# Kernel optimization log

Hardware: AMD Instinct MI355X
Metric: run time of the kernel (lower is better)

Reference implementation:

```python
import jax, jax.numpy as jnp
import numpy as np

B, D, L, N = 16, 256, 4096, 4096
MAX_SPAN = 64


def setup_inputs() -> dict:
    key = jax.random.key(0)
    k1, k2, k3 = jax.random.split(key, 3)
    features = jax.random.normal(k1, (B, D, L), dtype=jnp.float32)
    # TOI spans: start in [0, L - MAX_SPAN), length in [1, MAX_SPAN]
    start = jax.random.randint(k2, (B, N), 0, L - MAX_SPAN, dtype=jnp.int32)
    length = jax.random.randint(k3, (B, N), 1, MAX_SPAN + 1, dtype=jnp.int32)
    tois = jnp.stack([start, start + length], axis=-1)  # [B, N, 2]
    return {"features": features, "tois": tois}


def _pool_one(feat, toi):
    # feat: [D, L], toi: [N, 2] -> [N, 3*D]
    start = toi[:, 0]
    end = toi[:, 1]
    # cumsum with zero-padding column: [D, L+1]
    cs = jnp.concatenate(
        [jnp.zeros((feat.shape[0], 1), dtype=feat.dtype), jnp.cumsum(feat, axis=1)],
        axis=1,
    )
    span_len = (end - start).astype(feat.dtype)
    avg = (cs[:, end] - cs[:, start]) / span_len          # [D, N]
    head = feat[:, start]                                  # [D, N]
    tail = feat[:, end - 1]                                # [D, N]
    return jnp.concatenate([head, avg, tail], axis=0).T    # [N, 3*D]


def reference(features, tois):
    # features: [B, D, L] float32, tois: [B, N, 2] int32
    pooled = jax.vmap(_pool_one)(features, tois)           # [B, N, 3*D]
    out = pooled.reshape(-1, pooled.shape[-1])             # [B*N, 3*D]
    n = tois.shape[1]
    counts = jnp.cumsum(jnp.full((tois.shape[0],), n, dtype=jnp.int32))
    return out, counts
```

## Files before the change

### kernel.cpp

```cpp
#include <hip/hip_runtime.h>
#include <hip/hip_bf16.h>

constexpr int B = 16;
constexpr int D = 256;
constexpr int L = 4096;
constexpr int N = 4096;
constexpr int TS = 64;
constexpr int NT = L / TS;

__global__ __launch_bounds__(256) void tile_sums(const float* __restrict__ feat,
                                                 float* __restrict__ P) {
    int gw   = (blockIdx.x * blockDim.x + threadIdx.x) >> 6;
    int lane = threadIdx.x & 63;
    int row = gw >> 6;
    int t   = gw & 63;
    float v = feat[(size_t)row * L + t * TS + lane];
    #pragma unroll
    for (int off = 32; off > 0; off >>= 1) v += __shfl_xor(v, off, 64);
    if (lane == 0) P[gw] = v;
}

__global__ __launch_bounds__(256) void scan_partials(float* __restrict__ P,
                                                     float* __restrict__ cs_t) {
    int row = blockIdx.x * blockDim.x + threadIdx.x;
    if (row >= B * D) return;
    float run = 0.f;
    #pragma unroll
    for (int t = 0; t < NT; ++t) {
        float v = P[row * NT + t];
        P[row * NT + t] = run;
        run += v;
    }
    int b = row >> 8;
    int d = row & 255;
    cs_t[((size_t)b * (L + 1) + L) * D + d] = run;
}

__global__ __launch_bounds__(256) void transpose_scan(const float* __restrict__ feat,
                                                      const float* __restrict__ P,
                                                      float* __restrict__ cs_t) {
    __shared__ float tile[64][65];
    int bid = blockIdx.x;
    int t   = bid & 63;
    int dt  = (bid >> 6) & 3;
    int b   = bid >> 8;
    int tid = threadIdx.x;
    int ll  = tid & 63;
    int dd0 = tid >> 6;
    int d0  = dt * 64;
    int l0  = t * TS;

    #pragma unroll
    for (int k = 0; k < 16; ++k) {
        int dd = dd0 + k * 4;
        tile[dd][ll] = feat[((size_t)(b * D + d0 + dd)) * L + l0 + ll];
    }
    __syncthreads();

    if (tid < 64) {
        int dd  = tid;
        int row = b * D + d0 + dd;
        float run = P[row * NT + t];
        #pragma unroll
        for (int j = 0; j < TS; ++j) {
            float v = tile[dd][j];
            tile[dd][j] = run;
            run += v;
        }
    }
    __syncthreads();

    int dd  = tid & 63;
    int ll0 = tid >> 6;
    #pragma unroll
    for (int k = 0; k < 16; ++k) {
        int l = ll0 + k * 4;
        cs_t[((size_t)b * (L + 1) + l0 + l) * D + d0 + dd] = tile[dd][l];
    }
}

__global__ __launch_bounds__(256) void pool_queries(const float* __restrict__ cs_t,
                                                    const int* __restrict__ tois,
                                                    float* __restrict__ out) {
    int gw   = (blockIdx.x * blockDim.x + threadIdx.x) >> 6;
    int lane = threadIdx.x & 63;
    if (gw >= B * N) return;
    int b = gw >> 12;
    int s = tois[gw * 2 + 0];
    int e = tois[gw * 2 + 1];

    const size_t base = (size_t)b * (L + 1);
    const float4* r_s  = (const float4*)(cs_t + (base + s) * D);
    const float4* r_s1 = (const float4*)(cs_t + (base + s + 1) * D);
    const float4* r_e  = (const float4*)(cs_t + (base + e) * D);
    const float4* r_e1 = (const float4*)(cs_t + (base + e - 1) * D);

    float4 cs0 = r_s[lane];
    float4 cs1 = r_s1[lane];
    float4 ce0 = r_e[lane];
    float4 ce1 = r_e1[lane];

    float inv = 1.0f / (float)(e - s);
    float4 head = make_float4(cs1.x - cs0.x, cs1.y - cs0.y, cs1.z - cs0.z, cs1.w - cs0.w);
    float4 avg  = make_float4((ce0.x - cs0.x) * inv, (ce0.y - cs0.y) * inv,
                              (ce0.z - cs0.z) * inv, (ce0.w - cs0.w) * inv);
    float4 tail = make_float4(ce0.x - ce1.x, ce0.y - ce1.y, ce0.z - ce1.z, ce0.w - ce1.w);

    float* orow = out + (size_t)gw * (3 * D);
    ((float4*)orow)[lane]             = head;
    ((float4*)(orow + D))[lane]       = avg;
    ((float4*)(orow + 2 * D))[lane]   = tail;

    if (gw == 0 && lane < B)
        out[(size_t)B * N * (3 * D) + lane] = (float)((lane + 1) * N);
}

__global__ __launch_bounds__(256) void pool_direct(const float* __restrict__ feat,
                                                   const int* __restrict__ tois,
                                                   float* __restrict__ out) {
    int gw   = (blockIdx.x * blockDim.x + threadIdx.x) >> 6;
    int lane = threadIdx.x & 63;
    if (gw >= B * N) return;
    int b = gw >> 12;
    int s = tois[gw * 2 + 0];
    int e = tois[gw * 2 + 1];
    float inv = 1.0f / (float)(e - s);
    float* orow = out + (size_t)gw * (3 * D);
    #pragma unroll
    for (int c = 0; c < 4; ++c) {
        int d = c * 64 + lane;
        const float* f = feat + ((size_t)(b * D + d)) * L;
        float sum = 0.f;
        for (int j = s; j < e; ++j) sum += f[j];
        orow[d]         = f[s];
        orow[D + d]     = sum * inv;
        orow[2 * D + d] = f[e - 1];
    }
    if (gw == 0 && lane < B)
        out[(size_t)B * N * (3 * D) + lane] = (float)((lane + 1) * N);
}

extern "C" void kernel_launch(void* const* d_in, const int* in_sizes, int n_in,
                              void* d_out, int out_size, void* d_ws, size_t ws_size,
                              hipStream_t stream) {
    const float* feat = (const float*)d_in[0];
    const int*   tois = (const int*)d_in[1];
    float*       out  = (float*)d_out;

    const size_t cs_elems = (size_t)B * (L + 1) * D;
    const size_t p_elems  = (size_t)B * D * NT;
    const size_t need     = (cs_elems + p_elems) * sizeof(float);

    if (ws_size >= need) {
        float* cs_t = (float*)d_ws;
        float* P    = cs_t + cs_elems;

        tile_sums<<<B * D * NT / 4, 256, 0, stream>>>(feat, P);
        scan_partials<<<(B * D + 255) / 256, 256, 0, stream>>>(P, cs_t);
        transpose_scan<<<B * (D / 64) * NT, 256, 0, stream>>>(feat, P, cs_t);
        pool_queries<<<B * N / 4, 256, 0, stream>>>(cs_t, tois, out);
    } else {
        pool_direct<<<B * N / 4, 256, 0, stream>>>(feat, tois, out);
    }
}
```

Before: 322.2 us.

## Fuse tile sums and partial scan, parallelize tile scan, nontemporal output stores

Replaces the separate tile-sum and serial partial-scan kernels with one per-row kernel that reduces tiles with float4 loads and scans the 64 tile sums with a wavefront shuffle scan. The transpose kernel's single-wave serial 64-step scan becomes a parallel shuffle scan across all four wavefronts, with the offsets preloaded into shared memory. The pooling kernel uses vector-typed loads, int2 span loads and nontemporal stores for the large output write. The goal is to remove a kernel launch, the serial scan latency and cache pollution from the streaming output, at the cost of more shuffle instructions.

```diff
diff --git a/kernel.cpp b/kernel.cpp
--- a/kernel.cpp
+++ b/kernel.cpp
@@ -8,74 +8,88 @@
 constexpr int TS = 64;
 constexpr int NT = L / TS;
 
-__global__ __launch_bounds__(256) void tile_sums(const float* __restrict__ feat,
-                                                 float* __restrict__ P) {
-    int gw   = (blockIdx.x * blockDim.x + threadIdx.x) >> 6;
-    int lane = threadIdx.x & 63;
-    int row = gw >> 6;
-    int t   = gw & 63;
-    float v = feat[(size_t)row * L + t * TS + lane];
+typedef float v4f __attribute__((ext_vector_type(4)));
+
+__global__ __launch_bounds__(256) void row_scan(const float* __restrict__ feat,
+                                                float* __restrict__ P,
+                                                float* __restrict__ cs_t) {
+    __shared__ float tsum[NT];
+    int row = blockIdx.x;
+    int tid = threadIdx.x;
+    const float4* fr = (const float4*)(feat + (size_t)row * L);
+
+    float s[4];
     #pragma unroll
-    for (int off = 32; off > 0; off >>= 1) v += __shfl_xor(v, off, 64);
-    if (lane == 0) P[gw] = v;
-}
+    for (int r = 0; r < 4; ++r) {
+        float4 v = fr[r * 256 + tid];
+        s[r] = (v.x + v.y) + (v.z + v.w);
+    }
+    #pragma unroll
+    for (int r = 0; r < 4; ++r) {
+        float v = s[r];
+        #pragma unroll
+        for (int off = 1; off < 16; off <<= 1) v += __shfl_xor(v, off, 64);
+        if ((tid & 15) == 0) tsum[r * 16 + (tid >> 4)] = v;
+    }
+    __syncthreads();
 
-__global__ __launch_bounds__(256) void scan_partials(float* __restrict__ P,
-                                                     float* __restrict__ cs_t) {
-    int row = blockIdx.x * blockDim.x + threadIdx.x;
-    if (row >= B * D) return;
-    float run = 0.f;
-    #pragma unroll
-    for (int t = 0; t < NT; ++t) {
-        float v = P[row * NT + t];
-        P[row * NT + t] = run;
-        run += v;
+    if (tid < NT) {
+        float v = tsum[tid];
+        float incl = v;
+        #pragma unroll
+        for (int off = 1; off < 64; off <<= 1) {
+            float u = __shfl_up(incl, off, 64);
+            if (tid >= off) incl += u;
+        }
+        P[row * NT + tid] = incl - v;
+        if (tid == NT - 1) {
+            int b = row >> 8, d = row & 255;
+            cs_t[((size_t)b * (L + 1) + L) * D + d] = incl;
+        }
     }
-    int b = row >> 8;
-    int d = row & 255;
-    cs_t[((size_t)b * (L + 1) + L) * D + d] = run;
 }
 
 __global__ __launch_bounds__(256) void transpose_scan(const float* __restrict__ feat,
                                                       const float* __restrict__ P,
                                                       float* __restrict__ cs_t) {
     __shared__ float tile[64][65];
+    __shared__ float poff[64];
     int bid = blockIdx.x;
     int t   = bid & 63;
     int dt  = (bid >> 6) & 3;
     int b   = bid >> 8;
     int tid = threadIdx.x;
     int ll  = tid & 63;
-    int dd0 = tid >> 6;
+    int k0  = tid >> 6;
     int d0  = dt * 64;
     int l0  = t * TS;
 
+    if (tid < 64) poff[tid] = P[(b * D + d0 + tid) * NT + t];
     #pragma unroll
     for (int k = 0; k < 16; ++k) {
-        int dd = dd0 + k * 4;
+        int dd = k0 + k * 4;
         tile[dd][ll] = feat[((size_t)(b * D + d0 + dd)) * L + l0 + ll];
     }
     __syncthreads();
 
-    if (tid < 64) {
-        int dd  = tid;
-        int row = b * D + d0 + dd;
-        float run = P[row * NT + t];
+    #pragma unroll
+    for (int r = 0; r < 16; ++r) {
+        int dd = k0 * 16 + r;
+        float v = tile[dd][ll];
+        float incl = v;
         #pragma unroll
-        for (int j = 0; j < TS; ++j) {
-            float v = tile[dd][j];
-            tile[dd][j] = run;
-            run += v;
+        for (int off = 1; off < 64; off <<= 1) {
+            float u = __shfl_up(incl, off, 64);
+            if (ll >= off) incl += u;
         }
+        tile[dd][ll] = (incl - v) + poff[dd];
     }
     __syncthreads();
 
-    int dd  = tid & 63;
-    int ll0 = tid >> 6;
     #pragma unroll
     for (int k = 0; k < 16; ++k) {
-        int l = ll0 + k * 4;
-        cs_t[((size_t)b * (L + 1) + l0 + l) * D + d0 + dd] = tile[dd][l];
+        int l = k0 + k * 4;
+        cs_t[((size_t)b * (L + 1) + l0 + l) * D + d0 + ll] = tile[ll][l];
     }
 }
 
@@ -84,32 +98,28 @@
                                                     float* __restrict__ out) {
     int gw   = (blockIdx.x * blockDim.x + threadIdx.x) >> 6;
     int lane = threadIdx.x & 63;
-    if (gw >= B * N) return;
     int b = gw >> 12;
-    int s = tois[gw * 2 + 0];
-    int e = tois[gw * 2 + 1];
+    int2 se = ((const int2*)tois)[gw];
+    int s = se.x, e = se.y;
 
     const size_t base = (size_t)b * (L + 1);
-    const float4* r_s  = (const float4*)(cs_t + (base + s) * D);
-    const float4* r_s1 = (const float4*)(cs_t + (base + s + 1) * D);
-    const float4* r_e  = (const float4*)(cs_t + (base + e) * D);
-    const float4* r_e1 = (const float4*)(cs_t + (base + e - 1) * D);
+    const v4f* r_s = (const v4f*)(cs_t + (base + s) * D);
+    const v4f* r_e = (const v4f*)(cs_t + (base + e) * D);
 
-    float4 cs0 = r_s[lane];
-    float4 cs1 = r_s1[lane];
-    float4 ce0 = r_e[lane];
-    float4 ce1 = r_e1[lane];
+    v4f cs0 = r_s[lane];
+    v4f cs1 = r_s[lane + 64];
+    v4f ce1 = r_e[lane - 64];
+    v4f ce0 = r_e[lane];
 
     float inv = 1.0f / (float)(e - s);
-    float4 head = make_float4(cs1.x - cs0.x, cs1.y - cs0.y, cs1.z - cs0.z, cs1.w - cs0.w);
-    float4 avg  = make_float4((ce0.x - cs0.x) * inv, (ce0.y - cs0.y) * inv,
-                              (ce0.z - cs0.z) * inv, (ce0.w - cs0.w) * inv);
-    float4 tail = make_float4(ce0.x - ce1.x, ce0.y - ce1.y, ce0.z - ce1.z, ce0.w - ce1.w);
+    v4f head = cs1 - cs0;
+    v4f avg  = (ce0 - cs0) * inv;
+    v4f tail = ce0 - ce1;
 
-    float* orow = out + (size_t)gw * (3 * D);
-    ((float4*)orow)[lane]             = head;
-    ((float4*)(orow + D))[lane]       = avg;
-    ((float4*)(orow + 2 * D))[lane]   = tail;
+    v4f* orow = (v4f*)(out + (size_t)gw * (3 * D));
+    __builtin_nontemporal_store(head, orow + lane);
+    __builtin_nontemporal_store(avg,  orow + 64 + lane);
+    __builtin_nontemporal_store(tail, orow + 128 + lane);
 
     if (gw == 0 && lane < B)
         out[(size_t)B * N * (3 * D) + lane] = (float)((lane + 1) * N);
@@ -155,8 +165,7 @@
         float* cs_t = (float*)d_ws;
         float* P    = cs_t + cs_elems;
 
-        tile_sums<<<B * D * NT / 4, 256, 0, stream>>>(feat, P);
-        scan_partials<<<(B * D + 255) / 256, 256, 0, stream>>>(P, cs_t);
+        row_scan<<<B * D, 256, 0, stream>>>(feat, P, cs_t);
         transpose_scan<<<B * (D / 64) * NT, 256, 0, stream>>>(feat, P, cs_t);
         pool_queries<<<B * N / 4, 256, 0, stream>>>(cs_t, tois, out);
     } else {
```

Measured after the change: 292.3 us. 1.1x faster.
